# Kernel optimization log

Hardware: AMD Instinct MI355X
Metric: run time of the kernel (lower is better)

## Reference

```python
import jax, jax.numpy as jnp
import numpy as np

BS, SEQ, C = 8, 1024, 1024

def setup_inputs() -> dict:
    key = jax.random.key(0)
    ks = jax.random.split(key, 5)
    inp = {
        "input": jax.random.normal(ks[0], (BS, SEQ, C), dtype=jnp.float32),
        "Wq": jax.random.normal(ks[1], (C, C), dtype=jnp.float32) * 0.001,
        "Wk": jax.random.normal(ks[2], (C, C), dtype=jnp.float32) * 0.001,
        "Wv": jax.random.normal(ks[3], (C, C), dtype=jnp.float32) * 0.001,
        "bq": jnp.zeros((C,), dtype=jnp.float32),
        "bk": jnp.zeros((C,), dtype=jnp.float32),
        "bv": jnp.zeros((C,), dtype=jnp.float32),
        "bias_position": jnp.ones((SEQ, SEQ), dtype=jnp.float32),
    }
    return inp

def reference(input, Wq, Wk, Wv, bq, bk, bv, bias_position):
    # Linear layers (torch nn.Linear: x @ W.T + b)
    q = input @ Wq.T + bq                      # (bs, seq, c)
    k = input @ Wk.T + bk                      # (bs, seq, c)
    v = input @ Wv.T + bv                      # (bs, seq, c)
    # AFT: out[b,t,c] = sum_s exp(k[b,s,c] + bias[t,s]) * v[b,s,c]
    #                 / sum_s exp(k[b,s,c] + bias[t,s])
    # Factor exp(k + bias) = exp(bias) * exp(k) -> two GEMM-like einsums,
    # avoiding the (seq, bs, seq, c) intermediate of the original.
    ek = jnp.exp(k)                            # (bs, seq, c)
    eb = jnp.exp(bias_position)                # (t, s)
    numerator = jnp.einsum('ts,bsc->btc', eb, ek * v)   # (bs, t, c)
    denominator = jnp.einsum('ts,bsc->btc', eb, ek)     # (bs, t, c)
    out = jax.nn.sigmoid(q) * (numerator / denominator)
    return out
```

## Files before the change

kernel.cpp:

```cpp
#include <hip/hip_runtime.h>

#define BSZ 8
#define SEQL 1024
#define CHN 1024
#define M1 (BSZ*SEQL)

typedef __attribute__((ext_vector_type(8))) short bf16x8;
typedef __attribute__((ext_vector_type(4))) float f32x4;
typedef __attribute__((ext_vector_type(4))) unsigned short us4;
typedef __attribute__((ext_vector_type(8))) unsigned short us8;

static __device__ __forceinline__ unsigned short f2bf(float f){
  unsigned int u = __float_as_uint(f);
  u += 0x7fffu + ((u >> 16) & 1u);
  return (unsigned short)(u >> 16);
}
static __device__ __forceinline__ float bf2f(unsigned short h){
  return __uint_as_float(((unsigned int)h) << 16);
}
static __device__ __forceinline__ void gload16(const void* g, void* l){
  __builtin_amdgcn_global_load_lds((const __attribute__((address_space(1))) void*)g,
                                   (__attribute__((address_space(3))) void*)l,
                                   16, 0, 0);
}

#define SBAR() do { __builtin_amdgcn_sched_barrier(0); __builtin_amdgcn_s_barrier(); __builtin_amdgcn_sched_barrier(0); } while (0)
#define LGKM0() asm volatile("s_waitcnt lgkmcnt(0)" ::: "memory")
#define PRIO_HI() do { __builtin_amdgcn_s_setprio(1); __builtin_amdgcn_sched_barrier(0); } while (0)
#define PRIO_LO() do { __builtin_amdgcn_sched_barrier(0); __builtin_amdgcn_s_setprio(0); } while (0)

__global__ void prep_kernel(const float* __restrict__ x, const float* __restrict__ wq,
                            const float* __restrict__ wk, const float* __restrict__ wv,
                            const float* __restrict__ bias,
                            unsigned short* __restrict__ xb, unsigned short* __restrict__ wqb,
                            unsigned short* __restrict__ wkb, unsigned short* __restrict__ wvb,
                            unsigned short* __restrict__ ebb)
{
  const int NX = M1 * CHN;
  const int NW = CHN * CHN;
  const int total4 = (NX + 3 * NW + SEQL * SEQL) >> 2;
  for (int i = blockIdx.x * blockDim.x + threadIdx.x; i < total4;
       i += gridDim.x * blockDim.x) {
    int e = i << 2;
    const float* src; unsigned short* dst; int off; bool ex = false;
    if (e < NX)               { src = x;    dst = xb;  off = e; }
    else if (e < NX + NW)     { src = wq;   dst = wqb; off = e - NX; }
    else if (e < NX + 2 * NW) { src = wk;   dst = wkb; off = e - (NX + NW); }
    else if (e < NX + 3 * NW) { src = wv;   dst = wvb; off = e - (NX + 2 * NW); }
    else                      { src = bias; dst = ebb; off = e - (NX + 3 * NW); ex = true; }
    float4 v = *reinterpret_cast<const float4*>(src + off);
    if (ex) { v.x = expf(v.x); v.y = expf(v.y); v.z = expf(v.z); v.w = expf(v.w); }
    us4 o; o.x = f2bf(v.x); o.y = f2bf(v.y); o.z = f2bf(v.z); o.w = f2bf(v.w);
    *reinterpret_cast<us4*>(dst + off) = o;
  }
}

__global__ __launch_bounds__(512, 2) void gemm_qkv(
    const unsigned short* __restrict__ Xb,
    const unsigned short* __restrict__ Wq, const unsigned short* __restrict__ Wk,
    const unsigned short* __restrict__ Wv,
    const float* __restrict__ bq, const float* __restrict__ bk,
    const float* __restrict__ bv,
    unsigned short* __restrict__ Qb,
    unsigned short* __restrict__ EKT, unsigned short* __restrict__ EKVT)
{
  __shared__ unsigned short lds[2 * 20480];
  const int tid = threadIdx.x;
  const int lane = tid & 63;
  const int wid = tid >> 6;
  const int wm = wid >> 1;
  const int wn = wid & 1;
  const int nwg = gridDim.x;
  const int lid = blockIdx.x;
  const int sid = (lid & 7) * (nwg >> 3) + (lid >> 3);
  const int m0 = (sid >> 4) * 128;
  const int n0 = (sid & 15) * 64;

  const unsigned short* srcA[2]; int dA[2];
#pragma unroll
  for (int p = 0; p < 2; p++) {
    int l = p * 8192 + tid * 16;
    int row = l >> 7;
    int lc = ((l >> 4) & 7) ^ (row & 7);
    srcA[p] = Xb + (m0 + row) * CHN + lc * 8;
    dA[p] = l >> 1;
  }
  const unsigned short* srcB[3]; int dB[3];
  {
    int l = tid * 16;
    int row = l >> 7;
    int lc = ((l >> 4) & 7) ^ (row & 7);
#pragma unroll
    for (int w = 0; w < 3; w++) {
      const unsigned short* W = (w == 0) ? Wq : (w == 1) ? Wk : Wv;
      srcB[w] = W + (n0 + row) * CHN + lc * 8;
      dB[w] = 8192 + w * 4096 + (l >> 1);
    }
  }

  int aOff[2][2], bOff[2][2];
#pragma unroll
  for (int mi = 0; mi < 2; mi++) {
    int r = wm * 32 + mi * 16 + (lane & 15);
#pragma unroll
    for (int ks = 0; ks < 2; ks++)
      aOff[mi][ks] = r * 64 + ((((ks << 2) + (lane >> 4)) ^ (r & 7)) << 3);
  }
#pragma unroll
  for (int ni = 0; ni < 2; ni++) {
    int r = wn * 32 + ni * 16 + (lane & 15);
#pragma unroll
    for (int ks = 0; ks < 2; ks++)
      bOff[ni][ks] = r * 64 + ((((ks << 2) + (lane >> 4)) ^ (r & 7)) << 3);
  }

  f32x4 accq[2][2] = {}, acck[2][2] = {}, accv[2][2] = {};

#pragma unroll
  for (int p = 0; p < 2; p++) gload16(srcA[p], lds + dA[p]);
#pragma unroll
  for (int w = 0; w < 3; w++) gload16(srcB[w], lds + dB[w]);

  for (int t = 0; t < 16; ++t) {
    const int cur = (t & 1) * 20480;
    const int nxt = 20480 - cur;
    const int kn = (t + 1) << 6;
    if (t < 15) {
#pragma unroll
      for (int p = 0; p < 2; p++) gload16(srcA[p] + kn, lds + nxt + dA[p]);
      asm volatile("s_waitcnt vmcnt(2)" ::: "memory");
    } else {
      asm volatile("s_waitcnt vmcnt(0)" ::: "memory");
    }
    SBAR();
#pragma unroll
    for (int ks = 0; ks < 2; ks++) {
      bf16x8 af[2], bqf[2], bkf[2], bvf[2];
#pragma unroll
      for (int mi = 0; mi < 2; mi++)
        af[mi] = *reinterpret_cast<const bf16x8*>(lds + cur + aOff[mi][ks]);
#pragma unroll
      for (int ni = 0; ni < 2; ni++) {
        bqf[ni] = *reinterpret_cast<const bf16x8*>(lds + cur + 8192  + bOff[ni][ks]);
        bkf[ni] = *reinterpret_cast<const bf16x8*>(lds + cur + 12288 + bOff[ni][ks]);
        bvf[ni] = *reinterpret_cast<const bf16x8*>(lds + cur + 16384 + bOff[ni][ks]);
      }
      PRIO_HI();
#pragma unroll
      for (int ni = 0; ni < 2; ni++)
#pragma unroll
        for (int mi = 0; mi < 2; mi++) {
          accq[mi][ni] = __builtin_amdgcn_mfma_f32_16x16x32_bf16(af[mi], bqf[ni], accq[mi][ni], 0, 0, 0);
          acck[mi][ni] = __builtin_amdgcn_mfma_f32_16x16x32_bf16(af[mi], bkf[ni], acck[mi][ni], 0, 0, 0);
          accv[mi][ni] = __builtin_amdgcn_mfma_f32_16x16x32_bf16(af[mi], bvf[ni], accv[mi][ni], 0, 0, 0);
        }
      PRIO_LO();
      if (ks == 0 && t < 15) {
#pragma unroll
        for (int w = 0; w < 3; w++) gload16(srcB[w] + kn, lds + nxt + dB[w]);
      }
    }
    LGKM0();
    SBAR();
  }

  const int bIdx = m0 >> 10;
  const int s0 = m0 & 1023;
  const int rbq = (lane >> 4) * 4;
  float bqv[2], bkv[2], bvv[2];
#pragma unroll
  for (int ni = 0; ni < 2; ni++) {
    int c = n0 + wn * 32 + ni * 16 + (lane & 15);
    bqv[ni] = bq[c]; bkv[ni] = bk[c]; bvv[ni] = bv[c];
  }
#pragma unroll
  for (int mi = 0; mi < 2; mi++)
#pragma unroll
    for (int ni = 0; ni < 2; ni++) {
      int col = n0 + wn * 32 + ni * 16 + (lane & 15);
#pragma unroll
      for (int r = 0; r < 4; r++) {
        int mrow = m0 + wm * 32 + mi * 16 + rbq + r;
        Qb[mrow * CHN + col] = f2bf(accq[mi][ni][r] + bqv[ni]);
        float ekf = expf(acck[mi][ni][r] + bkv[ni]);
        acck[mi][ni][r] = ekf;
        accv[mi][ni][r] = ekf * (accv[mi][ni][r] + bvv[ni]);
      }
    }
#pragma unroll
  for (int mi = 0; mi < 2; mi++)
#pragma unroll
    for (int ni = 0; ni < 2; ni++) {
      int nloc = wn * 32 + ni * 16 + (lane & 15);
#pragma unroll
      for (int r = 0; r < 4; r++)
        lds[nloc * 136 + wm * 32 + mi * 16 + rbq + r] = f2bf(acck[mi][ni][r]);
    }
  __syncthreads();
#pragma unroll
  for (int it = 0; it < 2; it++) {
    int ch = it * 512 + tid;
    int nloc = ch >> 4, c8 = ch & 15;
    us8 v = *reinterpret_cast<const us8*>(lds + nloc * 136 + c8 * 8);
    *reinterpret_cast<us8*>(EKT + (bIdx * CHN + n0 + nloc) * SEQL + s0 + c8 * 8) = v;
  }
  __syncthreads();
#pragma unroll
  for (int mi = 0; mi < 2; mi++)
#pragma unroll
    for (int ni = 0; ni < 2; ni++) {
      int nloc = wn * 32 + ni * 16 + (lane & 15);
#pragma unroll
      for (int r = 0; r < 4; r++)
        lds[nloc * 136 + wm * 32 + mi * 16 + rbq + r] = f2bf(accv[mi][ni][r]);
    }
  __syncthreads();
#pragma unroll
  for (int it = 0; it < 2; it++) {
    int ch = it * 512 + tid;
    int nloc = ch >> 4, c8 = ch & 15;
    us8 v = *reinterpret_cast<const us8*>(lds + nloc * 136 + c8 * 8);
    *reinterpret_cast<us8*>(EKVT + (bIdx * CHN + n0 + nloc) * SEQL + s0 + c8 * 8) = v;
  }
}

__global__ __launch_bounds__(512, 4) void gemm_aft(
    const unsigned short* __restrict__ EB,
    const unsigned short* __restrict__ EKT, const unsigned short* __restrict__ EKVT,
    const unsigned short* __restrict__ Qb, float* __restrict__ out)
{
  __shared__ unsigned short lds[2 * 16384];
  const int tid = threadIdx.x;
  const int lane = tid & 63;
  const int wid = tid >> 6;
  const int wm = wid >> 1;
  const int wn = wid & 1;
  const int nwg = gridDim.x;
  const int lid = blockIdx.x;
  const int sid = (lid & 7) * (nwg >> 3) + (lid >> 3);
  const int t0 = (sid & 7) * 128;
  const int n0 = (sid >> 3) * 64;

  const unsigned short* srcA[2]; int dA[2];
#pragma unroll
  for (int p = 0; p < 2; p++) {
    int l = p * 8192 + tid * 16;
    int row = l >> 7;
    int lc = ((l >> 4) & 7) ^ (row & 7);
    srcA[p] = EB + (t0 + row) * SEQL + lc * 8;
    dA[p] = l >> 1;
  }
  const unsigned short* srcB[2]; int dB[2];
  {
    int l = tid * 16;
    int row = l >> 7;
    int lc = ((l >> 4) & 7) ^ (row & 7);
#pragma unroll
    for (int w = 0; w < 2; w++) {
      const unsigned short* B = (w == 0) ? EKT : EKVT;
      srcB[w] = B + (n0 + row) * SEQL + lc * 8;
      dB[w] = 8192 + w * 4096 + (l >> 1);
    }
  }

  int aOff[2][2], bOff[2][2];
#pragma unroll
  for (int mi = 0; mi < 2; mi++) {
    int r = wm * 32 + mi * 16 + (lane & 15);
#pragma unroll
    for (int ks = 0; ks < 2; ks++)
      aOff[mi][ks] = r * 64 + ((((ks << 2) + (lane >> 4)) ^ (r & 7)) << 3);
  }
#pragma unroll
  for (int ni = 0; ni < 2; ni++) {
    int r = wn * 32 + ni * 16 + (lane & 15);
#pragma unroll
    for (int ks = 0; ks < 2; ks++)
      bOff[ni][ks] = r * 64 + ((((ks << 2) + (lane >> 4)) ^ (r & 7)) << 3);
  }

  f32x4 accd[2][2] = {}, accn[2][2] = {};

#pragma unroll
  for (int p = 0; p < 2; p++) gload16(srcA[p], lds + dA[p]);
#pragma unroll
  for (int w = 0; w < 2; w++) gload16(srcB[w], lds + dB[w]);

  for (int t = 0; t < 16; ++t) {
    const int cur = (t & 1) * 16384;
    const int nxt = 16384 - cur;
    const int kn = (t + 1) << 6;
    if (t < 15) {
#pragma unroll
      for (int p = 0; p < 2; p++) gload16(srcA[p] + kn, lds + nxt + dA[p]);
      asm volatile("s_waitcnt vmcnt(2)" ::: "memory");
    } else {
      asm volatile("s_waitcnt vmcnt(0)" ::: "memory");
    }
    SBAR();
#pragma unroll
    for (int ks = 0; ks < 2; ks++) {
      bf16x8 af[2], bdf[2], bnf[2];
#pragma unroll
      for (int mi = 0; mi < 2; mi++)
        af[mi] = *reinterpret_cast<const bf16x8*>(lds + cur + aOff[mi][ks]);
#pragma unroll
      for (int ni = 0; ni < 2; ni++) {
        bdf[ni] = *reinterpret_cast<const bf16x8*>(lds + cur + 8192  + bOff[ni][ks]);
        bnf[ni] = *reinterpret_cast<const bf16x8*>(lds + cur + 12288 + bOff[ni][ks]);
      }
      PRIO_HI();
#pragma unroll
      for (int ni = 0; ni < 2; ni++)
#pragma unroll
        for (int mi = 0; mi < 2; mi++) {
          accd[mi][ni] = __builtin_amdgcn_mfma_f32_16x16x32_bf16(af[mi], bdf[ni], accd[mi][ni], 0, 0, 0);
          accn[mi][ni] = __builtin_amdgcn_mfma_f32_16x16x32_bf16(af[mi], bnf[ni], accn[mi][ni], 0, 0, 0);
        }
      PRIO_LO();
      if (ks == 0 && t < 15) {
#pragma unroll
        for (int w = 0; w < 2; w++) gload16(srcB[w] + kn, lds + nxt + dB[w]);
      }
    }
    LGKM0();
    SBAR();
  }

  const int rbq = (lane >> 4) * 4;
#pragma unroll
  for (int mi = 0; mi < 2; mi++)
#pragma unroll
    for (int ni = 0; ni < 2; ni++) {
      int nloc = wn * 32 + ni * 16 + (lane & 15);
      int n = n0 + nloc;
      int b = n >> 10, c = n & 1023;
#pragma unroll
      for (int r = 0; r < 4; r++) {
        int t = t0 + wm * 32 + mi * 16 + rbq + r;
        float qv = bf2f(Qb[(b * SEQL + t) * CHN + c]);
        float sig = 1.0f / (1.0f + expf(-qv));
        out[(b * SEQL + t) * CHN + c] = sig * accn[mi][ni][r] / accd[mi][ni][r];
      }
    }
}

extern "C" void kernel_launch(void* const* d_in, const int* in_sizes, int n_in,
                              void* d_out, int out_size, void* d_ws, size_t ws_size,
                              hipStream_t stream) {
  (void)in_sizes; (void)n_in; (void)out_size; (void)ws_size;
  const float* x    = (const float*)d_in[0];
  const float* wq   = (const float*)d_in[1];
  const float* wk   = (const float*)d_in[2];
  const float* wv   = (const float*)d_in[3];
  const float* bq   = (const float*)d_in[4];
  const float* bk   = (const float*)d_in[5];
  const float* bv   = (const float*)d_in[6];
  const float* bias = (const float*)d_in[7];
  float* out = (float*)d_out;

  char* ws = (char*)d_ws;
  const size_t MB = 1024 * 1024;
  unsigned short* Xb   = (unsigned short*)(ws);
  unsigned short* Wqb  = (unsigned short*)(ws + 16 * MB);
  unsigned short* Wkb  = (unsigned short*)(ws + 18 * MB);
  unsigned short* Wvb  = (unsigned short*)(ws + 20 * MB);
  unsigned short* EBb  = (unsigned short*)(ws + 22 * MB);
  unsigned short* Qb   = (unsigned short*)(ws + 24 * MB);
  unsigned short* EKT  = (unsigned short*)(ws + 40 * MB);
  unsigned short* EKVT = (unsigned short*)(ws + 56 * MB);

  prep_kernel<<<2048, 256, 0, stream>>>(x, wq, wk, wv, bias, Xb, Wqb, Wkb, Wvb, EBb);
  gemm_qkv<<<1024, 512, 0, stream>>>(Xb, Wqb, Wkb, Wvb, bq, bk, bv, Qb, EKT, EKVT);
  gemm_aft<<<1024, 512, 0, stream>>>(EBb, EKT, EKVT, Qb, out);
}
```

Before: 194.7 us.

## Enlarge GEMM block tiles in QKV and AFT kernels for more register reuse

```diff
diff --git a/kernel.cpp b/kernel.cpp
--- a/kernel.cpp
+++ b/kernel.cpp
@@ -64,7 +64,7 @@
     unsigned short* __restrict__ Qb,
     unsigned short* __restrict__ EKT, unsigned short* __restrict__ EKVT)
 {
-  __shared__ unsigned short lds[2 * 20480];
+  __shared__ unsigned short lds[2 * 28672];
   const int tid = threadIdx.x;
   const int lane = tid & 63;
   const int wid = tid >> 6;
@@ -73,12 +73,12 @@
   const int nwg = gridDim.x;
   const int lid = blockIdx.x;
   const int sid = (lid & 7) * (nwg >> 3) + (lid >> 3);
-  const int m0 = (sid >> 4) * 128;
+  const int m0 = (sid >> 4) * 256;
   const int n0 = (sid & 15) * 64;
 
-  const unsigned short* srcA[2]; int dA[2];
-#pragma unroll
-  for (int p = 0; p < 2; p++) {
+  const unsigned short* srcA[4]; int dA[4];
+#pragma unroll
+  for (int p = 0; p < 4; p++) {
     int l = p * 8192 + tid * 16;
     int row = l >> 7;
     int lc = ((l >> 4) & 7) ^ (row & 7);
@@ -94,14 +94,14 @@
     for (int w = 0; w < 3; w++) {
       const unsigned short* W = (w == 0) ? Wq : (w == 1) ? Wk : Wv;
       srcB[w] = W + (n0 + row) * CHN + lc * 8;
-      dB[w] = 8192 + w * 4096 + (l >> 1);
-    }
-  }
-
-  int aOff[2][2], bOff[2][2];
-#pragma unroll
-  for (int mi = 0; mi < 2; mi++) {
-    int r = wm * 32 + mi * 16 + (lane & 15);
+      dB[w] = 16384 + w * 4096 + (l >> 1);
+    }
+  }
+
+  int aOff[4][2], bOff[2][2];
+#pragma unroll
+  for (int mi = 0; mi < 4; mi++) {
+    int r = wm * 64 + mi * 16 + (lane & 15);
 #pragma unroll
     for (int ks = 0; ks < 2; ks++)
       aOff[mi][ks] = r * 64 + ((((ks << 2) + (lane >> 4)) ^ (r & 7)) << 3);
@@ -114,46 +114,45 @@
       bOff[ni][ks] = r * 64 + ((((ks << 2) + (lane >> 4)) ^ (r & 7)) << 3);
   }
 
-  f32x4 accq[2][2] = {}, acck[2][2] = {}, accv[2][2] = {};
-
-#pragma unroll
-  for (int p = 0; p < 2; p++) gload16(srcA[p], lds + dA[p]);
+  f32x4 accq[4][2] = {}, acck[4][2] = {}, accv[4][2] = {};
+
+#pragma unroll
+  for (int p = 0; p < 4; p++) gload16(srcA[p], lds + dA[p]);
 #pragma unroll
   for (int w = 0; w < 3; w++) gload16(srcB[w], lds + dB[w]);
 
   for (int t = 0; t < 16; ++t) {
-    const int cur = (t & 1) * 20480;
-    const int nxt = 20480 - cur;
+    const int cur = (t & 1) * 28672;
+    const int nxt = 28672 - cur;
     const int kn = (t + 1) << 6;
     if (t < 15) {
 #pragma unroll
-      for (int p = 0; p < 2; p++) gload16(srcA[p] + kn, lds + nxt + dA[p]);
-      asm volatile("s_waitcnt vmcnt(2)" ::: "memory");
+      for (int p = 0; p < 4; p++) gload16(srcA[p] + kn, lds + nxt + dA[p]);
+      asm volatile("s_waitcnt vmcnt(4)" ::: "memory");
     } else {
       asm volatile("s_waitcnt vmcnt(0)" ::: "memory");
     }
     SBAR();
 #pragma unroll
     for (int ks = 0; ks < 2; ks++) {
-      bf16x8 af[2], bqf[2], bkf[2], bvf[2];
-#pragma unroll
-      for (int mi = 0; mi < 2; mi++)
-        af[mi] = *reinterpret_cast<const bf16x8*>(lds + cur + aOff[mi][ks]);
+      bf16x8 bqf[2], bkf[2], bvf[2];
 #pragma unroll
       for (int ni = 0; ni < 2; ni++) {
-        bqf[ni] = *reinterpret_cast<const bf16x8*>(lds + cur + 8192  + bOff[ni][ks]);
-        bkf[ni] = *reinterpret_cast<const bf16x8*>(lds + cur + 12288 + bOff[ni][ks]);
-        bvf[ni] = *reinterpret_cast<const bf16x8*>(lds + cur + 16384 + bOff[ni][ks]);
+        bqf[ni] = *reinterpret_cast<const bf16x8*>(lds + cur + 16384 + bOff[ni][ks]);
+        bkf[ni] = *reinterpret_cast<const bf16x8*>(lds + cur + 20480 + bOff[ni][ks]);
+        bvf[ni] = *reinterpret_cast<const bf16x8*>(lds + cur + 24576 + bOff[ni][ks]);
       }
       PRIO_HI();
 #pragma unroll
-      for (int ni = 0; ni < 2; ni++)
-#pragma unroll
-        for (int mi = 0; mi < 2; mi++) {
-          accq[mi][ni] = __builtin_amdgcn_mfma_f32_16x16x32_bf16(af[mi], bqf[ni], accq[mi][ni], 0, 0, 0);
-          acck[mi][ni] = __builtin_amdgcn_mfma_f32_16x16x32_bf16(af[mi], bkf[ni], acck[mi][ni], 0, 0, 0);
-          accv[mi][ni] = __builtin_amdgcn_mfma_f32_16x16x32_bf16(af[mi], bvf[ni], accv[mi][ni], 0, 0, 0);
+      for (int mi = 0; mi < 4; mi++) {
+        bf16x8 af = *reinterpret_cast<const bf16x8*>(lds + cur + aOff[mi][ks]);
+#pragma unroll
+        for (int ni = 0; ni < 2; ni++) {
+          accq[mi][ni] = __builtin_amdgcn_mfma_f32_16x16x32_bf16(af, bqf[ni], accq[mi][ni], 0, 0, 0);
+          acck[mi][ni] = __builtin_amdgcn_mfma_f32_16x16x32_bf16(af, bkf[ni], acck[mi][ni], 0, 0, 0);
+          accv[mi][ni] = __builtin_amdgcn_mfma_f32_16x16x32_bf16(af, bvf[ni], accv[mi][ni], 0, 0, 0);
         }
+      }
       PRIO_LO();
       if (ks == 0 && t < 15) {
 #pragma unroll
@@ -174,13 +173,13 @@
     bqv[ni] = bq[c]; bkv[ni] = bk[c]; bvv[ni] = bv[c];
   }
 #pragma unroll
-  for (int mi = 0; mi < 2; mi++)
+  for (int mi = 0; mi < 4; mi++)
 #pragma unroll
     for (int ni = 0; ni < 2; ni++) {
       int col = n0 + wn * 32 + ni * 16 + (lane & 15);
 #pragma unroll
       for (int r = 0; r < 4; r++) {
-        int mrow = m0 + wm * 32 + mi * 16 + rbq + r;
+        int mrow = m0 + wm * 64 + mi * 16 + rbq + r;
         Qb[mrow * CHN + col] = f2bf(accq[mi][ni][r] + bqv[ni]);
         float ekf = expf(acck[mi][ni][r] + bkv[ni]);
         acck[mi][ni][r] = ekf;
@@ -188,85 +187,86 @@
       }
     }
 #pragma unroll
-  for (int mi = 0; mi < 2; mi++)
+  for (int mi = 0; mi < 4; mi++)
 #pragma unroll
     for (int ni = 0; ni < 2; ni++) {
       int nloc = wn * 32 + ni * 16 + (lane & 15);
 #pragma unroll
       for (int r = 0; r < 4; r++)
-        lds[nloc * 136 + wm * 32 + mi * 16 + rbq + r] = f2bf(acck[mi][ni][r]);
+        lds[nloc * 264 + wm * 64 + mi * 16 + rbq + r] = f2bf(acck[mi][ni][r]);
     }
   __syncthreads();
 #pragma unroll
-  for (int it = 0; it < 2; it++) {
+  for (int it = 0; it < 4; it++) {
     int ch = it * 512 + tid;
-    int nloc = ch >> 4, c8 = ch & 15;
-    us8 v = *reinterpret_cast<const us8*>(lds + nloc * 136 + c8 * 8);
+    int nloc = ch >> 5, c8 = ch & 31;
+    us8 v = *reinterpret_cast<const us8*>(lds + nloc * 264 + c8 * 8);
     *reinterpret_cast<us8*>(EKT + (bIdx * CHN + n0 + nloc) * SEQL + s0 + c8 * 8) = v;
   }
   __syncthreads();
 #pragma unroll
-  for (int mi = 0; mi < 2; mi++)
+  for (int mi = 0; mi < 4; mi++)
 #pragma unroll
     for (int ni = 0; ni < 2; ni++) {
       int nloc = wn * 32 + ni * 16 + (lane & 15);
 #pragma unroll
       for (int r = 0; r < 4; r++)
-        lds[nloc * 136 + wm * 32 + mi * 16 + rbq + r] = f2bf(accv[mi][ni][r]);
+        lds[nloc * 264 + wm * 64 + mi * 16 + rbq + r] = f2bf(accv[mi][ni][r]);
     }
   __syncthreads();
 #pragma unroll
-  for (int it = 0; it < 2; it++) {
+  for (int it = 0; it < 4; it++) {
     int ch = it * 512 + tid;
-    int nloc = ch >> 4, c8 = ch & 15;
-    us8 v = *reinterpret_cast<const us8*>(lds + nloc * 136 + c8 * 8);
+    int nloc = ch >> 5, c8 = ch & 31;
+    us8 v = *reinterpret_cast<const us8*>(lds + nloc * 264 + c8 * 8);
     *reinterpret_cast<us8*>(EKVT + (bIdx * CHN + n0 + nloc) * SEQL + s0 + c8 * 8) = v;
   }
 }
 
-__global__ __launch_bounds__(512, 4) void gemm_aft(
+__global__ __launch_bounds__(512, 2) void gemm_aft(
     const unsigned short* __restrict__ EB,
     const unsigned short* __restrict__ EKT, const unsigned short* __restrict__ EKVT,
     const unsigned short* __restrict__ Qb, float* __restrict__ out)
 {
-  __shared__ unsigned short lds[2 * 16384];
+  __shared__ unsigned short lds[2 * 32768];
   const int tid = threadIdx.x;
   const int lane = tid & 63;
   const int wid = tid >> 6;
-  const int wm = wid >> 1;
-  const int wn = wid & 1;
+  const int wm = wid >> 2;
+  const int wn = wid & 3;
   const int nwg = gridDim.x;
   const int lid = blockIdx.x;
   const int sid = (lid & 7) * (nwg >> 3) + (lid >> 3);
-  const int t0 = (sid & 7) * 128;
-  const int n0 = (sid >> 3) * 64;
-
-  const unsigned short* srcA[2]; int dA[2];
-#pragma unroll
-  for (int p = 0; p < 2; p++) {
+  const int t0 = (sid & 3) * 256;
+  const int n0 = (sid >> 2) * 128;
+
+  const unsigned short* srcA[4]; int dA[4];
+#pragma unroll
+  for (int p = 0; p < 4; p++) {
     int l = p * 8192 + tid * 16;
     int row = l >> 7;
     int lc = ((l >> 4) & 7) ^ (row & 7);
     srcA[p] = EB + (t0 + row) * SEQL + lc * 8;
     dA[p] = l >> 1;
   }
-  const unsigned short* srcB[2]; int dB[2];
-  {
-    int l = tid * 16;
-    int row = l >> 7;
-    int lc = ((l >> 4) & 7) ^ (row & 7);
-#pragma unroll
-    for (int w = 0; w < 2; w++) {
-      const unsigned short* B = (w == 0) ? EKT : EKVT;
-      srcB[w] = B + (n0 + row) * SEQL + lc * 8;
-      dB[w] = 8192 + w * 4096 + (l >> 1);
-    }
-  }
-
-  int aOff[2][2], bOff[2][2];
-#pragma unroll
-  for (int mi = 0; mi < 2; mi++) {
-    int r = wm * 32 + mi * 16 + (lane & 15);
+  const unsigned short* srcB[2][2]; int dB[2][2];
+#pragma unroll
+  for (int w = 0; w < 2; w++) {
+    const unsigned short* B = (w == 0) ? EKT : EKVT;
+#pragma unroll
+    for (int p = 0; p < 2; p++) {
+      int l = p * 8192 + tid * 16;
+      int row = l >> 7;
+      int lc = ((l >> 4) & 7) ^ (row & 7);
+      srcB[w][p] = B + (n0 + row) * SEQL + lc * 8;
+      dB[w][p] = 16384 + w * 8192 + (l >> 1);
+    }
+  }
+
+  int aOff[8][2], bOff[2][2];
+#pragma unroll
+  for (int mi = 0; mi < 8; mi++) {
+    int r = wm * 128 + mi * 16 + (lane & 15);
 #pragma unroll
     for (int ks = 0; ks < 2; ks++)
       aOff[mi][ks] = r * 64 + ((((ks << 2) + (lane >> 4)) ^ (r & 7)) << 3);
@@ -279,48 +279,51 @@
       bOff[ni][ks] = r * 64 + ((((ks << 2) + (lane >> 4)) ^ (r & 7)) << 3);
   }
 
-  f32x4 accd[2][2] = {}, accn[2][2] = {};
-
-#pragma unroll
-  for (int p = 0; p < 2; p++) gload16(srcA[p], lds + dA[p]);
-#pragma unroll
-  for (int w = 0; w < 2; w++) gload16(srcB[w], lds + dB[w]);
+  f32x4 accd[8][2] = {}, accn[8][2] = {};
+
+#pragma unroll
+  for (int p = 0; p < 4; p++) gload16(srcA[p], lds + dA[p]);
+#pragma unroll
+  for (int w = 0; w < 2; w++)
+#pragma unroll
+    for (int p = 0; p < 2; p++) gload16(srcB[w][p], lds + dB[w][p]);
 
   for (int t = 0; t < 16; ++t) {
-    const int cur = (t & 1) * 16384;
-    const int nxt = 16384 - cur;
+    const int cur = (t & 1) * 32768;
+    const int nxt = 32768 - cur;
     const int kn = (t + 1) << 6;
     if (t < 15) {
 #pragma unroll
-      for (int p = 0; p < 2; p++) gload16(srcA[p] + kn, lds + nxt + dA[p]);
-      asm volatile("s_waitcnt vmcnt(2)" ::: "memory");
+      for (int p = 0; p < 4; p++) gload16(srcA[p] + kn, lds + nxt + dA[p]);
+      asm volatile("s_waitcnt vmcnt(4)" ::: "memory");
     } else {
       asm volatile("s_waitcnt vmcnt(0)" ::: "memory");
     }
     SBAR();
 #pragma unroll
     for (int ks = 0; ks < 2; ks++) {
-      bf16x8 af[2], bdf[2], bnf[2];
-#pragma unroll
-      for (int mi = 0; mi < 2; mi++)
-        af[mi] = *reinterpret_cast<const bf16x8*>(lds + cur + aOff[mi][ks]);
+      bf16x8 bdf[2], bnf[2];
 #pragma unroll
       for (int ni = 0; ni < 2; ni++) {
-        bdf[ni] = *reinterpret_cast<const bf16x8*>(lds + cur + 8192  + bOff[ni][ks]);
-        bnf[ni] = *reinterpret_cast<const bf16x8*>(lds + cur + 12288 + bOff[ni][ks]);
+        bdf[ni] = *reinterpret_cast<const bf16x8*>(lds + cur + 16384 + bOff[ni][ks]);
+        bnf[ni] = *reinterpret_cast<const bf16x8*>(lds + cur + 24576 + bOff[ni][ks]);
       }
       PRIO_HI();
 #pragma unroll
-      for (int ni = 0; ni < 2; ni++)
-#pragma unroll
-        for (int mi = 0; mi < 2; mi++) {
-          accd[mi][ni] = __builtin_amdgcn_mfma_f32_16x16x32_bf16(af[mi], bdf[ni], accd[mi][ni], 0, 0, 0);
-          accn[mi][ni] = __builtin_amdgcn_mfma_f32_16x16x32_bf16(af[mi], bnf[ni], accn[mi][ni], 0, 0, 0);
+      for (int mi = 0; mi < 8; mi++) {
+        bf16x8 af = *reinterpret_cast<const bf16x8*>(lds + cur + aOff[mi][ks]);
+#pragma unroll
+        for (int ni = 0; ni < 2; ni++) {
+          accd[mi][ni] = __builtin_amdgcn_mfma_f32_16x16x32_bf16(af, bdf[ni], accd[mi][ni], 0, 0, 0);
+          accn[mi][ni] = __builtin_amdgcn_mfma_f32_16x16x32_bf16(af, bnf[ni], accn[mi][ni], 0, 0, 0);
         }
+      }
       PRIO_LO();
       if (ks == 0 && t < 15) {
 #pragma unroll
-        for (int w = 0; w < 2; w++) gload16(srcB[w] + kn, lds + nxt + dB[w]);
+        for (int w = 0; w < 2; w++)
+#pragma unroll
+          for (int p = 0; p < 2; p++) gload16(srcB[w][p] + kn, lds + nxt + dB[w][p]);
       }
     }
     LGKM0();
@@ -329,7 +332,7 @@
 
   const int rbq = (lane >> 4) * 4;
 #pragma unroll
-  for (int mi = 0; mi < 2; mi++)
+  for (int mi = 0; mi < 8; mi++)
 #pragma unroll
     for (int ni = 0; ni < 2; ni++) {
       int nloc = wn * 32 + ni * 16 + (lane & 15);
@@ -337,10 +340,10 @@
       int b = n >> 10, c = n & 1023;
 #pragma unroll
       for (int r = 0; r < 4; r++) {
-        int t = t0 + wm * 32 + mi * 16 + rbq + r;
-        float qv = bf2f(Qb[(b * SEQL + t) * CHN + c]);
+        int tt = t0 + wm * 128 + mi * 16 + rbq + r;
+        float qv = bf2f(Qb[(b * SEQL + tt) * CHN + c]);
         float sig = 1.0f / (1.0f + expf(-qv));
-        out[(b * SEQL + t) * CHN + c] = sig * accn[mi][ni][r] / accd[mi][ni][r];
+        out[(b * SEQL + tt) * CHN + c] = sig * accn[mi][ni][r] / accd[mi][ni][r];
       }
     }
 }
@@ -371,6 +374,6 @@
   unsigned short* EKVT = (unsigned short*)(ws + 56 * MB);
 
   prep_kernel<<<2048, 256, 0, stream>>>(x, wq, wk, wv, bias, Xb, Wqb, Wkb, Wvb, EBb);
-  gemm_qkv<<<1024, 512, 0, stream>>>(Xb, Wqb, Wkb, Wvb, bq, bk, bv, Qb, EKT, EKVT);
-  gemm_aft<<<1024, 512, 0, stream>>>(EBb, EKT, EKVT, Qb, out);
-}
+  gemm_qkv<<<512, 512, 0, stream>>>(Xb, Wqb, Wkb, Wvb, bq, bk, bv, Qb, EKT, EKVT);
+  gemm_aft<<<256, 512, 0, stream>>>(EBb, EKT, EKVT, Qb, out);
+}
```

Result: faster. 189.9 us (-2.5%).

## Enlarge QKV GEMM tile to 256 rows with per-matrix MFMA loop

Applied to the files above, without the earlier changes.

```diff
diff --git a/kernel.cpp b/kernel.cpp
--- a/kernel.cpp
+++ b/kernel.cpp
@@ -25,7 +25,7 @@
 }
 
 #define SBAR() do { __builtin_amdgcn_sched_barrier(0); __builtin_amdgcn_s_barrier(); __builtin_amdgcn_sched_barrier(0); } while (0)
-#define LGKM0() asm volatile("s_waitcnt lgkmcnt(0)" ::: "memory")
+#define LGKM0() do { asm volatile("s_waitcnt lgkmcnt(0)" ::: "memory"); __builtin_amdgcn_sched_barrier(0); } while (0)
 #define PRIO_HI() do { __builtin_amdgcn_s_setprio(1); __builtin_amdgcn_sched_barrier(0); } while (0)
 #define PRIO_LO() do { __builtin_amdgcn_sched_barrier(0); __builtin_amdgcn_s_setprio(0); } while (0)
 
@@ -64,162 +64,136 @@
     unsigned short* __restrict__ Qb,
     unsigned short* __restrict__ EKT, unsigned short* __restrict__ EKVT)
 {
-  __shared__ unsigned short lds[2 * 20480];
+  __shared__ unsigned short lds[2 * 28672];
   const int tid = threadIdx.x;
   const int lane = tid & 63;
   const int wid = tid >> 6;
-  const int wm = wid >> 1;
-  const int wn = wid & 1;
-  const int nwg = gridDim.x;
+  const int wm = wid >> 2;
+  const int wn = wid & 3;
   const int lid = blockIdx.x;
-  const int sid = (lid & 7) * (nwg >> 3) + (lid >> 3);
-  const int m0 = (sid >> 4) * 128;
+  const int sid = (lid & 7) * 64 + (lid >> 3);
+  const int m0 = (sid >> 4) * 256;
   const int n0 = (sid & 15) * 64;
 
-  const unsigned short* srcA[2]; int dA[2];
-#pragma unroll
-  for (int p = 0; p < 2; p++) {
+  const unsigned short* srcA[4]; int dA[4];
+#pragma unroll
+  for (int p = 0; p < 4; p++) {
     int l = p * 8192 + tid * 16;
     int row = l >> 7;
-    int lc = ((l >> 4) & 7) ^ (row & 7);
-    srcA[p] = Xb + (m0 + row) * CHN + lc * 8;
+    int ch = (l >> 4) & 7;
+    srcA[p] = Xb + (m0 + row) * CHN + (ch ^ (row & 7)) * 8;
     dA[p] = l >> 1;
   }
   const unsigned short* srcB[3]; int dB[3];
-  {
-    int l = tid * 16;
-    int row = l >> 7;
-    int lc = ((l >> 4) & 7) ^ (row & 7);
-#pragma unroll
-    for (int w = 0; w < 3; w++) {
-      const unsigned short* W = (w == 0) ? Wq : (w == 1) ? Wk : Wv;
-      srcB[w] = W + (n0 + row) * CHN + lc * 8;
-      dB[w] = 8192 + w * 4096 + (l >> 1);
-    }
-  }
-
-  int aOff[2][2], bOff[2][2];
-#pragma unroll
-  for (int mi = 0; mi < 2; mi++) {
-    int r = wm * 32 + mi * 16 + (lane & 15);
+#pragma unroll
+  for (int w = 0; w < 3; w++) {
+    int l = w * 8192 + tid * 16;
+    int brow = l >> 7;
+    int ch = (l >> 4) & 7;
+    const unsigned short* W = (w == 0) ? Wq : (w == 1) ? Wk : Wv;
+    srcB[w] = W + (n0 + (brow & 63)) * CHN + (ch ^ (brow & 7)) * 8;
+    dB[w] = 16384 + (l >> 1);
+  }
+
+  int aOff[8][2], bOff[3][2];
+#pragma unroll
+  for (int mi = 0; mi < 8; mi++) {
+    int r = wm * 128 + mi * 16 + (lane & 15);
 #pragma unroll
     for (int ks = 0; ks < 2; ks++)
       aOff[mi][ks] = r * 64 + ((((ks << 2) + (lane >> 4)) ^ (r & 7)) << 3);
   }
 #pragma unroll
-  for (int ni = 0; ni < 2; ni++) {
-    int r = wn * 32 + ni * 16 + (lane & 15);
+  for (int mat = 0; mat < 3; mat++) {
+    int r = mat * 64 + wn * 16 + (lane & 15);
 #pragma unroll
     for (int ks = 0; ks < 2; ks++)
-      bOff[ni][ks] = r * 64 + ((((ks << 2) + (lane >> 4)) ^ (r & 7)) << 3);
-  }
-
-  f32x4 accq[2][2] = {}, acck[2][2] = {}, accv[2][2] = {};
-
-#pragma unroll
-  for (int p = 0; p < 2; p++) gload16(srcA[p], lds + dA[p]);
+      bOff[mat][ks] = 16384 + r * 64 + ((((ks << 2) + (lane >> 4)) ^ (r & 7)) << 3);
+  }
+
+  f32x4 acc[3][8] = {};
+
+#pragma unroll
+  for (int p = 0; p < 4; p++) gload16(srcA[p], lds + dA[p]);
 #pragma unroll
   for (int w = 0; w < 3; w++) gload16(srcB[w], lds + dB[w]);
 
   for (int t = 0; t < 16; ++t) {
-    const int cur = (t & 1) * 20480;
-    const int nxt = 20480 - cur;
+    const int cur = (t & 1) * 28672;
+    const int nxt = 28672 - cur;
     const int kn = (t + 1) << 6;
     if (t < 15) {
 #pragma unroll
-      for (int p = 0; p < 2; p++) gload16(srcA[p] + kn, lds + nxt + dA[p]);
-      asm volatile("s_waitcnt vmcnt(2)" ::: "memory");
+      for (int p = 0; p < 4; p++) gload16(srcA[p] + kn, lds + nxt + dA[p]);
+#pragma unroll
+      for (int w = 0; w < 3; w++) gload16(srcB[w] + kn, lds + nxt + dB[w]);
+      asm volatile("s_waitcnt vmcnt(7)" ::: "memory");
     } else {
       asm volatile("s_waitcnt vmcnt(0)" ::: "memory");
     }
     SBAR();
 #pragma unroll
     for (int ks = 0; ks < 2; ks++) {
-      bf16x8 af[2], bqf[2], bkf[2], bvf[2];
-#pragma unroll
-      for (int mi = 0; mi < 2; mi++)
+      bf16x8 af[8];
+#pragma unroll
+      for (int mi = 0; mi < 8; mi++)
         af[mi] = *reinterpret_cast<const bf16x8*>(lds + cur + aOff[mi][ks]);
 #pragma unroll
-      for (int ni = 0; ni < 2; ni++) {
-        bqf[ni] = *reinterpret_cast<const bf16x8*>(lds + cur + 8192  + bOff[ni][ks]);
-        bkf[ni] = *reinterpret_cast<const bf16x8*>(lds + cur + 12288 + bOff[ni][ks]);
-        bvf[ni] = *reinterpret_cast<const bf16x8*>(lds + cur + 16384 + bOff[ni][ks]);
+      for (int mat = 0; mat < 3; mat++) {
+        bf16x8 bf = *reinterpret_cast<const bf16x8*>(lds + cur + bOff[mat][ks]);
+        LGKM0();
+        PRIO_HI();
+#pragma unroll
+        for (int mi = 0; mi < 8; mi++)
+          acc[mat][mi] = __builtin_amdgcn_mfma_f32_16x16x32_bf16(af[mi], bf, acc[mat][mi], 0, 0, 0);
+        PRIO_LO();
+        SBAR();
       }
-      PRIO_HI();
-#pragma unroll
-      for (int ni = 0; ni < 2; ni++)
-#pragma unroll
-        for (int mi = 0; mi < 2; mi++) {
-          accq[mi][ni] = __builtin_amdgcn_mfma_f32_16x16x32_bf16(af[mi], bqf[ni], accq[mi][ni], 0, 0, 0);
-          acck[mi][ni] = __builtin_amdgcn_mfma_f32_16x16x32_bf16(af[mi], bkf[ni], acck[mi][ni], 0, 0, 0);
-          accv[mi][ni] = __builtin_amdgcn_mfma_f32_16x16x32_bf16(af[mi], bvf[ni], accv[mi][ni], 0, 0, 0);
-        }
-      PRIO_LO();
-      if (ks == 0 && t < 15) {
-#pragma unroll
-        for (int w = 0; w < 3; w++) gload16(srcB[w] + kn, lds + nxt + dB[w]);
-      }
-    }
-    LGKM0();
-    SBAR();
+    }
   }
 
   const int bIdx = m0 >> 10;
   const int s0 = m0 & 1023;
   const int rbq = (lane >> 4) * 4;
-  float bqv[2], bkv[2], bvv[2];
-#pragma unroll
-  for (int ni = 0; ni < 2; ni++) {
-    int c = n0 + wn * 32 + ni * 16 + (lane & 15);
-    bqv[ni] = bq[c]; bkv[ni] = bk[c]; bvv[ni] = bv[c];
-  }
-#pragma unroll
-  for (int mi = 0; mi < 2; mi++)
-#pragma unroll
-    for (int ni = 0; ni < 2; ni++) {
-      int col = n0 + wn * 32 + ni * 16 + (lane & 15);
-#pragma unroll
-      for (int r = 0; r < 4; r++) {
-        int mrow = m0 + wm * 32 + mi * 16 + rbq + r;
-        Qb[mrow * CHN + col] = f2bf(accq[mi][ni][r] + bqv[ni]);
-        float ekf = expf(acck[mi][ni][r] + bkv[ni]);
-        acck[mi][ni][r] = ekf;
-        accv[mi][ni][r] = ekf * (accv[mi][ni][r] + bvv[ni]);
-      }
-    }
-#pragma unroll
-  for (int mi = 0; mi < 2; mi++)
-#pragma unroll
-    for (int ni = 0; ni < 2; ni++) {
-      int nloc = wn * 32 + ni * 16 + (lane & 15);
-#pragma unroll
-      for (int r = 0; r < 4; r++)
-        lds[nloc * 136 + wm * 32 + mi * 16 + rbq + r] = f2bf(acck[mi][ni][r]);
-    }
+  const int colLoc = wn * 16 + (lane & 15);
+  const float bqv = bq[n0 + colLoc];
+  const float bkv = bk[n0 + colLoc];
+  const float bvv = bv[n0 + colLoc];
+#pragma unroll
+  for (int mi = 0; mi < 8; mi++)
+#pragma unroll
+    for (int r = 0; r < 4; r++) {
+      int mrow = m0 + wm * 128 + mi * 16 + rbq + r;
+      Qb[mrow * CHN + n0 + colLoc] = f2bf(acc[0][mi][r] + bqv);
+      float ekf = expf(acc[1][mi][r] + bkv);
+      acc[1][mi][r] = ekf;
+      acc[2][mi][r] = ekf * (acc[2][mi][r] + bvv);
+    }
+#pragma unroll
+  for (int mi = 0; mi < 8; mi++)
+#pragma unroll
+    for (int r = 0; r < 4; r++)
+      lds[colLoc * 264 + wm * 128 + mi * 16 + rbq + r] = f2bf(acc[1][mi][r]);
   __syncthreads();
 #pragma unroll
-  for (int it = 0; it < 2; it++) {
+  for (int it = 0; it < 4; it++) {
     int ch = it * 512 + tid;
-    int nloc = ch >> 4, c8 = ch & 15;
-    us8 v = *reinterpret_cast<const us8*>(lds + nloc * 136 + c8 * 8);
+    int nloc = ch >> 5, c8 = ch & 31;
+    us8 v = *reinterpret_cast<const us8*>(lds + nloc * 264 + c8 * 8);
     *reinterpret_cast<us8*>(EKT + (bIdx * CHN + n0 + nloc) * SEQL + s0 + c8 * 8) = v;
   }
   __syncthreads();
 #pragma unroll
-  for (int mi = 0; mi < 2; mi++)
-#pragma unroll
-    for (int ni = 0; ni < 2; ni++) {
-      int nloc = wn * 32 + ni * 16 + (lane & 15);
-#pragma unroll
-      for (int r = 0; r < 4; r++)
-        lds[nloc * 136 + wm * 32 + mi * 16 + rbq + r] = f2bf(accv[mi][ni][r]);
-    }
+  for (int mi = 0; mi < 8; mi++)
+#pragma unroll
+    for (int r = 0; r < 4; r++)
+      lds[colLoc * 264 + wm * 128 + mi * 16 + rbq + r] = f2bf(acc[2][mi][r]);
   __syncthreads();
 #pragma unroll
-  for (int it = 0; it < 2; it++) {
+  for (int it = 0; it < 4; it++) {
     int ch = it * 512 + tid;
-    int nloc = ch >> 4, c8 = ch & 15;
-    us8 v = *reinterpret_cast<const us8*>(lds + nloc * 136 + c8 * 8);
+    int nloc = ch >> 5, c8 = ch & 31;
+    us8 v = *reinterpret_cast<const us8*>(lds + nloc * 264 + c8 * 8);
     *reinterpret_cast<us8*>(EKVT + (bIdx * CHN + n0 + nloc) * SEQL + s0 + c8 * 8) = v;
   }
 }
@@ -371,6 +345,6 @@
   unsigned short* EKVT = (unsigned short*)(ws + 56 * MB);
 
   prep_kernel<<<2048, 256, 0, stream>>>(x, wq, wk, wv, bias, Xb, Wqb, Wkb, Wvb, EBb);
-  gemm_qkv<<<1024, 512, 0, stream>>>(Xb, Wqb, Wkb, Wvb, bq, bk, bv, Qb, EKT, EKVT);
+  gemm_qkv<<<512, 512, 0, stream>>>(Xb, Wqb, Wkb, Wvb, bq, bk, bv, Qb, EKT, EKVT);
   gemm_aft<<<1024, 512, 0, stream>>>(EBb, EKT, EKVT, Qb, out);
 }
```

Result: slower. 199.2 us (+2.4%).
